# Performance work log

Measured on AMD Instinct MI355X. Metric: run time of the kernel, lower is better.

Reference implementation:

```python
import jax, jax.numpy as jnp
import numpy as np

N = 50000      # nodes
E = 800000     # edges (before self loops)
F_DIM = 512    # raw feature dim
HID = 64       # hidden dim (= per-head dim, concat=False)
HEADS = 4
EMB = 64
NEG_SLOPE = 0.2
LN_EPS = 1e-5


def setup_inputs() -> dict:
    key = jax.random.key(0)
    ks = jax.random.split(key, 24)
    rn = lambda k, shape: jax.random.normal(k, shape, dtype=jnp.float32) * 0.05
    inp = {
        'features': jax.random.normal(ks[0], (N, F_DIM), dtype=jnp.float32),
        'edge_index': jax.random.randint(ks[1], (2, E), 0, N),
        'Wt': rn(ks[2], (F_DIM, HID)), 'bt': jnp.zeros((HID,), jnp.float32),
        'Wp': rn(ks[3], (HID, EMB)), 'bp': jnp.zeros((EMB,), jnp.float32),
    }
    for l in range(2):
        o = 4 + l * 4
        inp[f'Wg{l}'] = rn(ks[o], (HID, HEADS * HID))
        inp[f'as{l}'] = rn(ks[o + 1], (HEADS, HID))
        inp[f'ad{l}'] = rn(ks[o + 2], (HEADS, HID))
        inp[f'bg{l}'] = jnp.zeros((HID,), jnp.float32)
        inp[f'g{l}'] = jnp.ones((HID,), jnp.float32)
        inp[f'b{l}'] = jnp.zeros((HID,), jnp.float32)
        inp[f'a{l}'] = jnp.full((1,), 0.25, jnp.float32)  # PReLU weight
    return inp


def gat_block(x, src, dst, Wg, a_src, a_dst, bg, gamma, beta, prelu_a):
    # GATConv (heads=HEADS, concat=False, add_self_loops already in src/dst)
    h = (x @ Wg).reshape(N, HEADS, HID)                    # [N,H,C]
    al_s = jnp.einsum('nhc,hc->nh', h, a_src)              # [N,H]
    al_d = jnp.einsum('nhc,hc->nh', h, a_dst)
    e = jax.nn.leaky_relu(al_s[src] + al_d[dst], NEG_SLOPE)  # [E,H]
    m = jax.ops.segment_max(e, dst, num_segments=N)
    ex = jnp.exp(e - m[dst])
    denom = jax.ops.segment_sum(ex, dst, num_segments=N)
    alpha = ex / denom[dst]                                # segment softmax over in-edges
    out = jax.ops.segment_sum(h[src] * alpha[:, :, None], dst, num_segments=N)  # [N,H,C]
    out = out.mean(axis=1) + bg                            # concat=False -> mean heads
    # LayerNorm
    mu = out.mean(-1, keepdims=True)
    var = ((out - mu) ** 2).mean(-1, keepdims=True)
    xn = (out - mu) / jnp.sqrt(var + LN_EPS) * gamma + beta
    # PReLU
    return jnp.where(xn > 0, xn, prelu_a * xn)


def reference(features, edge_index, Wt, bt, Wp, bp,
              Wg0, as0, ad0, bg0, g0, b0, a0,
              Wg1, as1, ad1, bg1, g1, b1, a1):
    loops = jnp.arange(N)
    src = jnp.concatenate([edge_index[0], loops])
    dst = jnp.concatenate([edge_index[1], loops])
    x = features @ Wt + bt
    x = x + gat_block(x, src, dst, Wg0, as0, ad0, bg0, g0, b0, a0)
    x = x + gat_block(x, src, dst, Wg1, as1, ad1, bg1, g1, b1, a1)
    z = x @ Wp + bp
    return z / jnp.maximum(jnp.linalg.norm(z, axis=-1, keepdims=True), 1e-12)
```

## Files before the change

### kernel.cpp

```cpp
#include <hip/hip_runtime.h>
#include <hip/hip_bf16.h>

typedef __attribute__((ext_vector_type(8))) short bvec8;
typedef __attribute__((ext_vector_type(4))) float fvec4;

__device__ __forceinline__ void splitf(float f, short& hi, short& lo) {
  __hip_bfloat16 h = __float2bfloat16(f);
  float r = f - __bfloat162float(h);
  __hip_bfloat16 l = __float2bfloat16(r);
  hi = *(short*)&h;
  lo = *(short*)&l;
}
__device__ __forceinline__ float bits2f(unsigned short u) {
  unsigned int v = ((unsigned int)u) << 16;
  return __uint_as_float(v);
}

__global__ void k_degree(const int* __restrict__ ei, int* __restrict__ cnt, int E, int N) {
  int i = blockIdx.x * 256 + threadIdx.x;
  if (i >= E + N) return;
  int d = (i < E) ? ei[E + i] : (i - E);
  atomicAdd(&cnt[d], 1);
}

__global__ __launch_bounds__(1024) void k_scan_blk(const int* __restrict__ cnt, int* __restrict__ off,
                                                   int* __restrict__ bsum, int N) {
  __shared__ int wsum[16];
  int t = threadIdx.x, lane = t & 63, wv = t >> 6;
  int idx = blockIdx.x * 4096 + t * 4;
  int4 v = make_int4(0, 0, 0, 0);
  if (idx < N) v = *(const int4*)(cnt + idx);
  int s0 = v.x, s1 = s0 + v.y, s2 = s1 + v.z, s3 = s2 + v.w;
  int sc = s3;
  #pragma unroll
  for (int d = 1; d < 64; d <<= 1) {
    int u = __shfl_up(sc, d, 64);
    if (lane >= d) sc += u;
  }
  if (lane == 63) wsum[wv] = sc;
  __syncthreads();
  int woff = 0;
  #pragma unroll
  for (int w = 0; w < 16; ++w) woff += (w < wv) ? wsum[w] : 0;
  int eb = woff + sc - s3;
  if (idx < N) {
    int4 o = make_int4(eb, eb + s0, eb + s1, eb + s2);
    *(int4*)(off + idx) = o;
  }
  if (t == 1023) bsum[blockIdx.x] = woff + sc;
}

__global__ __launch_bounds__(1024) void k_scan_add(int* __restrict__ off, int* __restrict__ cur,
                                                   const int* __restrict__ bsum, int total, int N) {
  int t = threadIdx.x;
  if (blockIdx.x == 0 && t == 0) off[N] = total;
  int b = 0;
  for (int i = 0; i < blockIdx.x; ++i) b += bsum[i];
  int idx = blockIdx.x * 4096 + t * 4;
  if (idx >= N) return;
  int4 o = *(const int4*)(off + idx);
  o.x += b; o.y += b; o.z += b; o.w += b;
  *(int4*)(off + idx) = o;
  *(int4*)(cur + idx) = o;
}

__global__ void k_scatter(const int* __restrict__ ei, int* __restrict__ cur, int* __restrict__ csr, int E, int N) {
  int i = blockIdx.x * 256 + threadIdx.x;
  if (i >= E + N) return;
  int s, d;
  if (i < E) { s = ei[i]; d = ei[E + i]; } else { s = i - E; d = i - E; }
  int p = atomicAdd(&cur[d], 1);
  csr[p] = s;
}

__global__ __launch_bounds__(64) void k_prep(const float* __restrict__ Wg0, const float* __restrict__ Wg1,
                                             const float* __restrict__ Wt,
                                             short* __restrict__ pk0, short* __restrict__ pk1,
                                             short* __restrict__ wtpk) {
  int b = blockIdx.x;
  int lane = threadIdx.x;
  int fq = lane >> 4, fr = lane & 15;
  bvec8 hv, lv;
  if (b < 64) {
    const float* Wg = (b < 32) ? Wg0 : Wg1;
    short* pk = (b < 32) ? pk0 : pk1;
    int tile = b & 31;
    int w = tile >> 3, s = (tile >> 2) & 1, ct = tile & 3;
    #pragma unroll
    for (int j = 0; j < 8; ++j) {
      short hh, ll;
      splitf(Wg[(size_t)(s * 32 + fq * 8 + j) * 256 + w * 64 + ct * 16 + fr], hh, ll);
      hv[j] = hh; lv[j] = ll;
    }
    *(bvec8*)(pk + tile * 1024 + lane * 8) = hv;
    *(bvec8*)(pk + tile * 1024 + 512 + lane * 8) = lv;
  } else {
    int tile = b - 64;
    int s = tile >> 2, nt = tile & 3;
    #pragma unroll
    for (int j = 0; j < 8; ++j) {
      short hh, ll;
      splitf(Wt[(size_t)(s * 32 + fq * 8 + j) * 64 + nt * 16 + fr], hh, ll);
      hv[j] = hh; lv[j] = ll;
    }
    *(bvec8*)(wtpk + tile * 1024 + lane * 8) = hv;
    *(bvec8*)(wtpk + tile * 1024 + 512 + lane * 8) = lv;
  }
}

__global__ __launch_bounds__(256) void k_x0(const float* __restrict__ feat, const short* __restrict__ wtpk,
                                            const float* __restrict__ bt,
                                            short* __restrict__ xhi, short* __restrict__ xlo, int N) {
  const int t = threadIdx.x;
  const int lane = t & 63;
  const int w = t >> 6;
  const int fr = lane & 15;
  const int fq = lane >> 4;
  const int n0 = blockIdx.x * 128;

  int ar0 = n0 + w * 32 + fr;      if (ar0 >= N) ar0 = N - 1;
  int ar1 = n0 + w * 32 + 16 + fr; if (ar1 >= N) ar1 = N - 1;
  const float* fb0 = feat + (size_t)ar0 * 512 + fq * 8;
  const float* fb1 = feat + (size_t)ar1 * 512 + fq * 8;

  fvec4 acc[2][4];
  #pragma unroll
  for (int m = 0; m < 2; ++m)
    #pragma unroll
    for (int nt = 0; nt < 4; ++nt) acc[m][nt] = (fvec4){0.f, 0.f, 0.f, 0.f};

  for (int s = 0; s < 16; ++s) {
    bvec8 bh[4], bl[4];
    #pragma unroll
    for (int nt = 0; nt < 4; ++nt) {
      bh[nt] = *(const bvec8*)(wtpk + (s * 4 + nt) * 1024 + lane * 8);
      bl[nt] = *(const bvec8*)(wtpk + (s * 4 + nt) * 1024 + 512 + lane * 8);
    }
    #pragma unroll
    for (int m = 0; m < 2; ++m) {
      const float* fb = m ? fb1 : fb0;
      float4 f0 = *(const float4*)(fb + s * 32);
      float4 f1 = *(const float4*)(fb + s * 32 + 4);
      float fv[8] = {f0.x, f0.y, f0.z, f0.w, f1.x, f1.y, f1.z, f1.w};
      bvec8 ah, al;
      #pragma unroll
      for (int j = 0; j < 8; ++j) { short hh, ll; splitf(fv[j], hh, ll); ah[j] = hh; al[j] = ll; }
      #pragma unroll
      for (int nt = 0; nt < 4; ++nt) {
        acc[m][nt] = __builtin_amdgcn_mfma_f32_16x16x32_bf16(ah, bh[nt], acc[m][nt], 0, 0, 0);
        acc[m][nt] = __builtin_amdgcn_mfma_f32_16x16x32_bf16(ah, bl[nt], acc[m][nt], 0, 0, 0);
        acc[m][nt] = __builtin_amdgcn_mfma_f32_16x16x32_bf16(al, bh[nt], acc[m][nt], 0, 0, 0);
      }
    }
  }
  #pragma unroll
  for (int m = 0; m < 2; ++m)
    #pragma unroll
    for (int nt = 0; nt < 4; ++nt) {
      float btv = bt[nt * 16 + fr];
      #pragma unroll
      for (int r = 0; r < 4; ++r) {
        int node = n0 + w * 32 + m * 16 + fq * 4 + r;
        if (node < N) {
          short hh, ll;
          splitf(acc[m][nt][r] + btv, hh, ll);
          xhi[(size_t)node * 64 + nt * 16 + fr] = hh;
          xlo[(size_t)node * 64 + nt * 16 + fr] = ll;
        }
      }
    }
}

__global__ __launch_bounds__(256) void k_h(const short* __restrict__ xhi, const short* __restrict__ xlo,
                                           const short* __restrict__ pk,
                                           const float* __restrict__ as_, const float* __restrict__ ad_,
                                           signed char* __restrict__ h8, float2* __restrict__ alsc,
                                           float* __restrict__ ald, int N) {
  const int t = threadIdx.x;
  const int lane = t & 63;
  const int w = t >> 6;
  const int fr = lane & 15;
  const int fq = lane >> 4;
  const int n0 = blockIdx.x * 64;

  bvec8 bh[2][4], bl[2][4];
  #pragma unroll
  for (int s = 0; s < 2; ++s)
    #pragma unroll
    for (int ct = 0; ct < 4; ++ct) {
      int tile = (w * 2 + s) * 4 + ct;
      bh[s][ct] = *(const bvec8*)(pk + tile * 1024 + lane * 8);
      bl[s][ct] = *(const bvec8*)(pk + tile * 1024 + 512 + lane * 8);
    }
  fvec4 acc[4][4];
  #pragma unroll
  for (int nt = 0; nt < 4; ++nt)
    #pragma unroll
    for (int ct = 0; ct < 4; ++ct) acc[nt][ct] = (fvec4){0.f, 0.f, 0.f, 0.f};
  #pragma unroll
  for (int nt = 0; nt < 4; ++nt) {
    int row = n0 + nt * 16 + fr; if (row >= N) row = N - 1;
    const short* xh = xhi + (size_t)row * 64 + fq * 8;
    const short* xl = xlo + (size_t)row * 64 + fq * 8;
    #pragma unroll
    for (int s = 0; s < 2; ++s) {
      const bvec8 ah = *(const bvec8*)(xh + s * 32);
      const bvec8 al = *(const bvec8*)(xl + s * 32);
      #pragma unroll
      for (int ct = 0; ct < 4; ++ct) {
        acc[nt][ct] = __builtin_amdgcn_mfma_f32_16x16x32_bf16(ah, bh[s][ct], acc[nt][ct], 0, 0, 0);
        acc[nt][ct] = __builtin_amdgcn_mfma_f32_16x16x32_bf16(ah, bl[s][ct], acc[nt][ct], 0, 0, 0);
        acc[nt][ct] = __builtin_amdgcn_mfma_f32_16x16x32_bf16(al, bh[s][ct], acc[nt][ct], 0, 0, 0);
      }
    }
  }
  float asv[4], adv[4];
  #pragma unroll
  for (int ct = 0; ct < 4; ++ct) {
    asv[ct] = as_[w * 64 + ct * 16 + fr];
    adv[ct] = ad_[w * 64 + ct * 16 + fr];
  }
  #pragma unroll
  for (int nt = 0; nt < 4; ++nt) {
    #pragma unroll
    for (int r = 0; r < 4; ++r) {
      int n = n0 + nt * 16 + fq * 4 + r;
      float ps = 0.f, pd = 0.f;
      float rmax = 0.f;
      #pragma unroll
      for (int ct = 0; ct < 4; ++ct) {
        float av = acc[nt][ct][r];
        ps = fmaf(av, asv[ct], ps);
        pd = fmaf(av, adv[ct], pd);
        rmax = fmaxf(rmax, fabsf(av));
      }
      #pragma unroll
      for (int m = 1; m < 16; m <<= 1) {
        ps += __shfl_xor(ps, m, 64);
        pd += __shfl_xor(pd, m, 64);
        rmax = fmaxf(rmax, __shfl_xor(rmax, m, 64));
      }
      float scale = rmax * (1.f / 127.f);
      float qinv = rmax > 0.f ? 127.f / rmax : 0.f;
      if (fr == 0 && n < N) {
        alsc[(size_t)n * 4 + w] = make_float2(ps, scale);
        ald[(size_t)n * 4 + w] = pd;
      }
      if (n < N) {
        #pragma unroll
        for (int ct = 0; ct < 4; ++ct) {
          int iv = __float2int_rn(acc[nt][ct][r] * qinv);
          h8[(size_t)n * 256 + w * 64 + ct * 16 + fr] = (signed char)iv;
        }
      }
    }
  }
}

template <bool FINAL>
__global__ __launch_bounds__(256) void k_agg(const signed char* __restrict__ h8, const float2* __restrict__ alsc,
                                             const float* __restrict__ ald, const int* __restrict__ off,
                                             const int* __restrict__ csr, const float* __restrict__ bg,
                                             const float* __restrict__ gam, const float* __restrict__ bet,
                                             const float* __restrict__ pa,
                                             short* __restrict__ xhi, short* __restrict__ xlo,
                                             const float* __restrict__ Wp, const float* __restrict__ bp,
                                             float* __restrict__ out, int N) {
  int lane = threadIdx.x & 63;
  int n = blockIdx.x * 4 + (threadIdx.x >> 6);
  if (n >= N) return;
  int hh = lane >> 4;
  int cg = (lane & 15) * 4;
  float aldv = ald[(size_t)n * 4 + hh];
  int e0 = __builtin_amdgcn_readfirstlane(off[n]);
  int e1 = __builtin_amdgcn_readfirstlane(off[n + 1]);
  float a0 = 0, a1 = 0, a2 = 0, a3 = 0, den = 0;
  const int co = hh * 64 + cg;
  int e = e0;
  for (; e + 4 <= e1; e += 4) {
    int s0 = csr[e + 0], s1 = csr[e + 1], s2 = csr[e + 2], s3 = csr[e + 3];
    float2 p0 = alsc[(size_t)s0 * 4 + hh];
    float2 p1 = alsc[(size_t)s1 * 4 + hh];
    float2 p2 = alsc[(size_t)s2 * 4 + hh];
    float2 p3 = alsc[(size_t)s3 * 4 + hh];
    uchar4 g0 = *(const uchar4*)(h8 + (size_t)s0 * 256 + co);
    uchar4 g1 = *(const uchar4*)(h8 + (size_t)s1 * 256 + co);
    uchar4 g2 = *(const uchar4*)(h8 + (size_t)s2 * 256 + co);
    uchar4 g3 = *(const uchar4*)(h8 + (size_t)s3 * 256 + co);
    float t0 = p0.x + aldv; t0 = fmaxf(t0, 0.2f * t0); float w0 = __expf(t0);
    float t1 = p1.x + aldv; t1 = fmaxf(t1, 0.2f * t1); float w1 = __expf(t1);
    float t2 = p2.x + aldv; t2 = fmaxf(t2, 0.2f * t2); float w2 = __expf(t2);
    float t3 = p3.x + aldv; t3 = fmaxf(t3, 0.2f * t3); float w3 = __expf(t3);
    den += (w0 + w1) + (w2 + w3);
    float ws0 = w0 * p0.y, ws1 = w1 * p1.y, ws2 = w2 * p2.y, ws3 = w3 * p3.y;
    a0 += ws0 * (float)(signed char)g0.x + ws1 * (float)(signed char)g1.x
        + ws2 * (float)(signed char)g2.x + ws3 * (float)(signed char)g3.x;
    a1 += ws0 * (float)(signed char)g0.y + ws1 * (float)(signed char)g1.y
        + ws2 * (float)(signed char)g2.y + ws3 * (float)(signed char)g3.y;
    a2 += ws0 * (float)(signed char)g0.z + ws1 * (float)(signed char)g1.z
        + ws2 * (float)(signed char)g2.z + ws3 * (float)(signed char)g3.z;
    a3 += ws0 * (float)(signed char)g0.w + ws1 * (float)(signed char)g1.w
        + ws2 * (float)(signed char)g2.w + ws3 * (float)(signed char)g3.w;
  }
  for (; e < e1; ++e) {
    int s = csr[e];
    float2 p = alsc[(size_t)s * 4 + hh];
    float t = p.x + aldv;
    t = fmaxf(t, 0.2f * t);
    float w = __expf(t);
    den += w;
    float ws = w * p.y;
    uchar4 g = *(const uchar4*)(h8 + (size_t)s * 256 + co);
    a0 += ws * (float)(signed char)g.x;
    a1 += ws * (float)(signed char)g.y;
    a2 += ws * (float)(signed char)g.z;
    a3 += ws * (float)(signed char)g.w;
  }
  float inv = 1.0f / den;
  a0 *= inv; a1 *= inv; a2 *= inv; a3 *= inv;
  a0 += __shfl_xor(a0, 16, 64); a0 += __shfl_xor(a0, 32, 64);
  a1 += __shfl_xor(a1, 16, 64); a1 += __shfl_xor(a1, 32, 64);
  a2 += __shfl_xor(a2, 16, 64); a2 += __shfl_xor(a2, 32, 64);
  a3 += __shfl_xor(a3, 16, 64); a3 += __shfl_xor(a3, 32, 64);
  float v0 = a0 * 0.25f + bg[cg + 0];
  float v1 = a1 * 0.25f + bg[cg + 1];
  float v2 = a2 * 0.25f + bg[cg + 2];
  float v3 = a3 * 0.25f + bg[cg + 3];
  float sum = v0 + v1 + v2 + v3;
  #pragma unroll
  for (int m = 1; m < 16; m <<= 1) sum += __shfl_xor(sum, m, 64);
  float mu = sum * (1.f / 64.f);
  float d0 = v0 - mu, d1 = v1 - mu, d2 = v2 - mu, d3 = v3 - mu;
  float vv = d0 * d0 + d1 * d1 + d2 * d2 + d3 * d3;
  #pragma unroll
  for (int m = 1; m < 16; m <<= 1) vv += __shfl_xor(vv, m, 64);
  float rstd = rsqrtf(vv * (1.f / 64.f) + 1e-5f);
  float A = pa[0];
  float y0 = d0 * rstd * gam[cg + 0] + bet[cg + 0];
  float y1 = d1 * rstd * gam[cg + 1] + bet[cg + 1];
  float y2 = d2 * rstd * gam[cg + 2] + bet[cg + 2];
  float y3 = d3 * rstd * gam[cg + 3] + bet[cg + 3];
  y0 = y0 > 0.f ? y0 : A * y0;
  y1 = y1 > 0.f ? y1 : A * y1;
  y2 = y2 > 0.f ? y2 : A * y2;
  y3 = y3 > 0.f ? y3 : A * y3;
  float o0 = 0.f, o1 = 0.f, o2 = 0.f, o3 = 0.f;
  if (lane < 16) {
    ushort4 xh = *(const ushort4*)((const unsigned short*)xhi + (size_t)n * 64 + cg);
    ushort4 xl = *(const ushort4*)((const unsigned short*)xlo + (size_t)n * 64 + cg);
    o0 = bits2f(xh.x) + bits2f(xl.x) + y0;
    o1 = bits2f(xh.y) + bits2f(xl.y) + y1;
    o2 = bits2f(xh.z) + bits2f(xl.z) + y2;
    o3 = bits2f(xh.w) + bits2f(xl.w) + y3;
  }
  if (!FINAL) {
    if (lane < 16) {
      short h0, l0, h1, l1, h2, l2, h3, l3;
      splitf(o0, h0, l0); splitf(o1, h1, l1); splitf(o2, h2, l2); splitf(o3, h3, l3);
      ushort4 oh = make_ushort4((unsigned short)h0, (unsigned short)h1, (unsigned short)h2, (unsigned short)h3);
      ushort4 ol = make_ushort4((unsigned short)l0, (unsigned short)l1, (unsigned short)l2, (unsigned short)l3);
      *(ushort4*)((unsigned short*)xhi + (size_t)n * 64 + cg) = oh;
      *(ushort4*)((unsigned short*)xlo + (size_t)n * 64 + cg) = ol;
    }
  } else {
    float acc = bp[lane];
    #pragma unroll
    for (int g = 0; g < 16; ++g) {
      float rx = __shfl(o0, g, 64), ry = __shfl(o1, g, 64);
      float rz = __shfl(o2, g, 64), rw = __shfl(o3, g, 64);
      const float* wp = Wp + g * 4 * 64 + lane;
      acc = fmaf(rx, wp[0],   acc);
      acc = fmaf(ry, wp[64],  acc);
      acc = fmaf(rz, wp[128], acc);
      acc = fmaf(rw, wp[192], acc);
    }
    float sq = acc * acc;
    #pragma unroll
    for (int m = 1; m < 64; m <<= 1) sq += __shfl_xor(sq, m, 64);
    float nrm = fmaxf(sqrtf(sq), 1e-12f);
    out[(size_t)n * 64 + lane] = acc / nrm;
  }
}

extern "C" void kernel_launch(void* const* d_in, const int* in_sizes, int n_in,
                              void* d_out, int out_size, void* d_ws, size_t ws_size,
                              hipStream_t stream) {
  const float* feat = (const float*)d_in[0];
  const int*   ei   = (const int*)d_in[1];
  const float* Wt   = (const float*)d_in[2];
  const float* bt   = (const float*)d_in[3];
  const float* Wp   = (const float*)d_in[4];
  const float* bp   = (const float*)d_in[5];
  const float* Wg[2]  = {(const float*)d_in[6],  (const float*)d_in[13]};
  const float* as_[2] = {(const float*)d_in[7],  (const float*)d_in[14]};
  const float* ad_[2] = {(const float*)d_in[8],  (const float*)d_in[15]};
  const float* bg[2]  = {(const float*)d_in[9],  (const float*)d_in[16]};
  const float* gm[2]  = {(const float*)d_in[10], (const float*)d_in[17]};
  const float* be[2]  = {(const float*)d_in[11], (const float*)d_in[18]};
  const float* pa[2]  = {(const float*)d_in[12], (const float*)d_in[19]};

  const int N = in_sizes[0] / 512;
  const int E = in_sizes[1] / 2;

  short* xhi = (short*)d_ws;
  short* xlo = xhi + (size_t)N * 64;
  signed char* h8 = (signed char*)(xlo + (size_t)N * 64);
  float2* alsc = (float2*)(h8 + (size_t)N * 256);
  float* ald = (float*)(alsc + (size_t)N * 4);
  int* cnt = (int*)(ald + (size_t)N * 4);
  int* cur = cnt + N;
  int* csr = cur + N;
  int* off = csr + (E + N);
  int* bsum = off + (N + 1);
  short* pk0 = (short*)(((uintptr_t)(bsum + 16) + 15) & ~(uintptr_t)15);
  short* pk1 = pk0 + 32768;
  short* wtpk = pk1 + 32768;

  hipMemsetAsync(cnt, 0, (size_t)N * sizeof(int), stream);
  int eb = (E + N + 255) / 256;
  int SB = (N + 4095) / 4096;
  k_degree<<<eb, 256, 0, stream>>>(ei, cnt, E, N);
  k_prep<<<128, 64, 0, stream>>>(Wg[0], Wg[1], Wt, pk0, pk1, wtpk);
  k_scan_blk<<<SB, 1024, 0, stream>>>(cnt, off, bsum, N);
  k_scan_add<<<SB, 1024, 0, stream>>>(off, cur, bsum, E + N, N);
  k_scatter<<<eb, 256, 0, stream>>>(ei, cur, csr, E, N);

  int nb4 = (N + 3) / 4;
  int nb64 = (N + 63) / 64;
  int nb128 = (N + 127) / 128;
  k_x0<<<nb128, 256, 0, stream>>>(feat, wtpk, bt, xhi, xlo, N);

  k_h<<<nb64, 256, 0, stream>>>(xhi, xlo, pk0, as_[0], ad_[0], h8, alsc, ald, N);
  k_agg<false><<<nb4, 256, 0, stream>>>(h8, alsc, ald, off, csr, bg[0], gm[0], be[0], pa[0],
                                        xhi, xlo, Wp, bp, (float*)d_out, N);
  k_h<<<nb64, 256, 0, stream>>>(xhi, xlo, pk1, as_[1], ad_[1], h8, alsc, ald, N);
  k_agg<true><<<nb4, 256, 0, stream>>>(h8, alsc, ald, off, csr, bg[1], gm[1], be[1], pa[1],
                                       xhi, xlo, Wp, bp, (float*)d_out, N);
}
```

Baseline: 476.6 us.

## Split edges across lane groups and gather full int8 rows with 16-byte loads

The aggregation kernel's work mapping changes. Each group of 16 lanes now handles a different in-edge and reads a whole 256-byte int8 row with 16-byte vector loads, instead of every lane reading 4 bytes of each edge row in turn. Partial sums are then combined across edge groups and across heads with cross-lane shuffles before LayerNorm, PReLU and the residual. This cuts the number of gather instructions per edge and processes 8 edges per iteration. In exchange, each lane holds 16 accumulators, adds reduction shuffles and a masked tail loop, and the kernel gets a minimum-occupancy hint of 6 blocks.

```diff
diff --git a/kernel.cpp b/kernel.cpp
--- a/kernel.cpp
+++ b/kernel.cpp
@@ -3,6 +3,8 @@
 
 typedef __attribute__((ext_vector_type(8))) short bvec8;
 typedef __attribute__((ext_vector_type(4))) float fvec4;
+typedef __attribute__((ext_vector_type(16))) unsigned char ucvec16;
+typedef __attribute__((ext_vector_type(8))) unsigned short usvec8;
 
 __device__ __forceinline__ void splitf(float f, short& hi, short& lo) {
   __hip_bfloat16 h = __float2bfloat16(f);
@@ -258,121 +260,121 @@
 }
 
 template <bool FINAL>
-__global__ __launch_bounds__(256) void k_agg(const signed char* __restrict__ h8, const float2* __restrict__ alsc,
-                                             const float* __restrict__ ald, const int* __restrict__ off,
-                                             const int* __restrict__ csr, const float* __restrict__ bg,
-                                             const float* __restrict__ gam, const float* __restrict__ bet,
-                                             const float* __restrict__ pa,
-                                             short* __restrict__ xhi, short* __restrict__ xlo,
-                                             const float* __restrict__ Wp, const float* __restrict__ bp,
-                                             float* __restrict__ out, int N) {
-  int lane = threadIdx.x & 63;
-  int n = blockIdx.x * 4 + (threadIdx.x >> 6);
+__global__ __launch_bounds__(256, 6) void k_agg(const signed char* __restrict__ h8, const float2* __restrict__ alsc,
+                                                const float* __restrict__ ald, const int* __restrict__ off,
+                                                const int* __restrict__ csr, const float* __restrict__ bg,
+                                                const float* __restrict__ gam, const float* __restrict__ bet,
+                                                const float* __restrict__ pa,
+                                                short* __restrict__ xhi, short* __restrict__ xlo,
+                                                const float* __restrict__ Wp, const float* __restrict__ bp,
+                                                float* __restrict__ out, int N) {
+  const int lane = threadIdx.x & 63;
+  const int n = blockIdx.x * 4 + (threadIdx.x >> 6);
   if (n >= N) return;
-  int hh = lane >> 4;
-  int cg = (lane & 15) * 4;
-  float aldv = ald[(size_t)n * 4 + hh];
+  const int g = lane >> 4;
+  const int r = lane & 15;
+  const int hd = r >> 2;
+  const int c0 = (r & 3) * 16;
+
+  float aldv = ald[(size_t)n * 4 + hd];
   int e0 = __builtin_amdgcn_readfirstlane(off[n]);
   int e1 = __builtin_amdgcn_readfirstlane(off[n + 1]);
-  float a0 = 0, a1 = 0, a2 = 0, a3 = 0, den = 0;
-  const int co = hh * 64 + cg;
+  float a[16];
+  #pragma unroll
+  for (int k = 0; k < 16; ++k) a[k] = 0.f;
+  float den = 0.f;
+
   int e = e0;
-  for (; e + 4 <= e1; e += 4) {
-    int s0 = csr[e + 0], s1 = csr[e + 1], s2 = csr[e + 2], s3 = csr[e + 3];
-    float2 p0 = alsc[(size_t)s0 * 4 + hh];
-    float2 p1 = alsc[(size_t)s1 * 4 + hh];
-    float2 p2 = alsc[(size_t)s2 * 4 + hh];
-    float2 p3 = alsc[(size_t)s3 * 4 + hh];
-    uchar4 g0 = *(const uchar4*)(h8 + (size_t)s0 * 256 + co);
-    uchar4 g1 = *(const uchar4*)(h8 + (size_t)s1 * 256 + co);
-    uchar4 g2 = *(const uchar4*)(h8 + (size_t)s2 * 256 + co);
-    uchar4 g3 = *(const uchar4*)(h8 + (size_t)s3 * 256 + co);
-    float t0 = p0.x + aldv; t0 = fmaxf(t0, 0.2f * t0); float w0 = __expf(t0);
-    float t1 = p1.x + aldv; t1 = fmaxf(t1, 0.2f * t1); float w1 = __expf(t1);
-    float t2 = p2.x + aldv; t2 = fmaxf(t2, 0.2f * t2); float w2 = __expf(t2);
-    float t3 = p3.x + aldv; t3 = fmaxf(t3, 0.2f * t3); float w3 = __expf(t3);
-    den += (w0 + w1) + (w2 + w3);
-    float ws0 = w0 * p0.y, ws1 = w1 * p1.y, ws2 = w2 * p2.y, ws3 = w3 * p3.y;
-    a0 += ws0 * (float)(signed char)g0.x + ws1 * (float)(signed char)g1.x
-        + ws2 * (float)(signed char)g2.x + ws3 * (float)(signed char)g3.x;
-    a1 += ws0 * (float)(signed char)g0.y + ws1 * (float)(signed char)g1.y
-        + ws2 * (float)(signed char)g2.y + ws3 * (float)(signed char)g3.y;
-    a2 += ws0 * (float)(signed char)g0.z + ws1 * (float)(signed char)g1.z
-        + ws2 * (float)(signed char)g2.z + ws3 * (float)(signed char)g3.z;
-    a3 += ws0 * (float)(signed char)g0.w + ws1 * (float)(signed char)g1.w
-        + ws2 * (float)(signed char)g2.w + ws3 * (float)(signed char)g3.w;
-  }
-  for (; e < e1; ++e) {
-    int s = csr[e];
-    float2 p = alsc[(size_t)s * 4 + hh];
-    float t = p.x + aldv;
-    t = fmaxf(t, 0.2f * t);
-    float w = __expf(t);
+  for (; e + 8 <= e1; e += 8) {
+    int sA = csr[e + g];
+    int sB = csr[e + 4 + g];
+    ucvec16 rowA = *(const ucvec16*)(h8 + (size_t)sA * 256 + r * 16);
+    ucvec16 rowB = *(const ucvec16*)(h8 + (size_t)sB * 256 + r * 16);
+    float2 pA = alsc[(size_t)sA * 4 + hd];
+    float2 pB = alsc[(size_t)sB * 4 + hd];
+    float tA = pA.x + aldv; tA = fmaxf(tA, 0.2f * tA); float wA = __expf(tA);
+    float tB = pB.x + aldv; tB = fmaxf(tB, 0.2f * tB); float wB = __expf(tB);
+    den += wA + wB;
+    float wsA = wA * pA.y, wsB = wB * pB.y;
+    #pragma unroll
+    for (int k = 0; k < 16; ++k) {
+      a[k] = fmaf(wsA, (float)(signed char)rowA[k], a[k]);
+      a[k] = fmaf(wsB, (float)(signed char)rowB[k], a[k]);
+    }
+  }
+  for (; e < e1; e += 4) {
+    int idx = e + g;
+    bool act = idx < e1;
+    int s = csr[act ? idx : (e1 - 1)];
+    ucvec16 row = *(const ucvec16*)(h8 + (size_t)s * 256 + r * 16);
+    float2 p = alsc[(size_t)s * 4 + hd];
+    float t = p.x + aldv; t = fmaxf(t, 0.2f * t);
+    float w = act ? __expf(t) : 0.f;
     den += w;
     float ws = w * p.y;
-    uchar4 g = *(const uchar4*)(h8 + (size_t)s * 256 + co);
-    a0 += ws * (float)(signed char)g.x;
-    a1 += ws * (float)(signed char)g.y;
-    a2 += ws * (float)(signed char)g.z;
-    a3 += ws * (float)(signed char)g.w;
+    #pragma unroll
+    for (int k = 0; k < 16; ++k) a[k] = fmaf(ws, (float)(signed char)row[k], a[k]);
+  }
+
+  den += __shfl_xor(den, 16, 64); den += __shfl_xor(den, 32, 64);
+  #pragma unroll
+  for (int k = 0; k < 16; ++k) {
+    a[k] += __shfl_xor(a[k], 16, 64);
+    a[k] += __shfl_xor(a[k], 32, 64);
   }
   float inv = 1.0f / den;
-  a0 *= inv; a1 *= inv; a2 *= inv; a3 *= inv;
-  a0 += __shfl_xor(a0, 16, 64); a0 += __shfl_xor(a0, 32, 64);
-  a1 += __shfl_xor(a1, 16, 64); a1 += __shfl_xor(a1, 32, 64);
-  a2 += __shfl_xor(a2, 16, 64); a2 += __shfl_xor(a2, 32, 64);
-  a3 += __shfl_xor(a3, 16, 64); a3 += __shfl_xor(a3, 32, 64);
-  float v0 = a0 * 0.25f + bg[cg + 0];
-  float v1 = a1 * 0.25f + bg[cg + 1];
-  float v2 = a2 * 0.25f + bg[cg + 2];
-  float v3 = a3 * 0.25f + bg[cg + 3];
-  float sum = v0 + v1 + v2 + v3;
-  #pragma unroll
-  for (int m = 1; m < 16; m <<= 1) sum += __shfl_xor(sum, m, 64);
-  float mu = sum * (1.f / 64.f);
-  float d0 = v0 - mu, d1 = v1 - mu, d2 = v2 - mu, d3 = v3 - mu;
-  float vv = d0 * d0 + d1 * d1 + d2 * d2 + d3 * d3;
-  #pragma unroll
-  for (int m = 1; m < 16; m <<= 1) vv += __shfl_xor(vv, m, 64);
-  float rstd = rsqrtf(vv * (1.f / 64.f) + 1e-5f);
+  #pragma unroll
+  for (int k = 0; k < 16; ++k) {
+    a[k] *= inv;
+    a[k] += __shfl_xor(a[k], 4, 64);
+    a[k] += __shfl_xor(a[k], 8, 64);
+  }
+  float v[16];
+  float psum = 0.f;
+  #pragma unroll
+  for (int k = 0; k < 16; ++k) {
+    v[k] = a[k] * 0.25f + bg[c0 + k];
+    psum += v[k];
+  }
+  psum += __shfl_xor(psum, 1, 64); psum += __shfl_xor(psum, 2, 64);
+  float mu = psum * (1.f / 64.f);
+  float pvar = 0.f;
+  #pragma unroll
+  for (int k = 0; k < 16; ++k) { float d = v[k] - mu; pvar += d * d; }
+  pvar += __shfl_xor(pvar, 1, 64); pvar += __shfl_xor(pvar, 2, 64);
+  float rstd = rsqrtf(pvar * (1.f / 64.f) + 1e-5f);
   float A = pa[0];
-  float y0 = d0 * rstd * gam[cg + 0] + bet[cg + 0];
-  float y1 = d1 * rstd * gam[cg + 1] + bet[cg + 1];
-  float y2 = d2 * rstd * gam[cg + 2] + bet[cg + 2];
-  float y3 = d3 * rstd * gam[cg + 3] + bet[cg + 3];
-  y0 = y0 > 0.f ? y0 : A * y0;
-  y1 = y1 > 0.f ? y1 : A * y1;
-  y2 = y2 > 0.f ? y2 : A * y2;
-  y3 = y3 > 0.f ? y3 : A * y3;
-  float o0 = 0.f, o1 = 0.f, o2 = 0.f, o3 = 0.f;
-  if (lane < 16) {
-    ushort4 xh = *(const ushort4*)((const unsigned short*)xhi + (size_t)n * 64 + cg);
-    ushort4 xl = *(const ushort4*)((const unsigned short*)xlo + (size_t)n * 64 + cg);
-    o0 = bits2f(xh.x) + bits2f(xl.x) + y0;
-    o1 = bits2f(xh.y) + bits2f(xl.y) + y1;
-    o2 = bits2f(xh.z) + bits2f(xl.z) + y2;
-    o3 = bits2f(xh.w) + bits2f(xl.w) + y3;
+  float o[16];
+  {
+    const unsigned short* xh = (const unsigned short*)xhi + (size_t)n * 64 + c0;
+    const unsigned short* xl = (const unsigned short*)xlo + (size_t)n * 64 + c0;
+    #pragma unroll
+    for (int k = 0; k < 16; ++k) {
+      float y = (v[k] - mu) * rstd * gam[c0 + k] + bet[c0 + k];
+      y = y > 0.f ? y : A * y;
+      o[k] = bits2f(xh[k]) + bits2f(xl[k]) + y;
+    }
   }
   if (!FINAL) {
-    if (lane < 16) {
-      short h0, l0, h1, l1, h2, l2, h3, l3;
-      splitf(o0, h0, l0); splitf(o1, h1, l1); splitf(o2, h2, l2); splitf(o3, h3, l3);
-      ushort4 oh = make_ushort4((unsigned short)h0, (unsigned short)h1, (unsigned short)h2, (unsigned short)h3);
-      ushort4 ol = make_ushort4((unsigned short)l0, (unsigned short)l1, (unsigned short)l2, (unsigned short)l3);
-      *(ushort4*)((unsigned short*)xhi + (size_t)n * 64 + cg) = oh;
-      *(ushort4*)((unsigned short*)xlo + (size_t)n * 64 + cg) = ol;
+    if (lane < 4) {
+      unsigned short oh[16], ol[16];
+      #pragma unroll
+      for (int k = 0; k < 16; ++k) {
+        short hh, ll; splitf(o[k], hh, ll);
+        oh[k] = (unsigned short)hh; ol[k] = (unsigned short)ll;
+      }
+      #pragma unroll
+      for (int q = 0; q < 2; ++q) {
+        *(usvec8*)((unsigned short*)xhi + (size_t)n * 64 + c0 + q * 8) = *(usvec8*)(oh + q * 8);
+        *(usvec8*)((unsigned short*)xlo + (size_t)n * 64 + c0 + q * 8) = *(usvec8*)(ol + q * 8);
+      }
     }
   } else {
     float acc = bp[lane];
     #pragma unroll
-    for (int g = 0; g < 16; ++g) {
-      float rx = __shfl(o0, g, 64), ry = __shfl(o1, g, 64);
-      float rz = __shfl(o2, g, 64), rw = __shfl(o3, g, 64);
-      const float* wp = Wp + g * 4 * 64 + lane;
-      acc = fmaf(rx, wp[0],   acc);
-      acc = fmaf(ry, wp[64],  acc);
-      acc = fmaf(rz, wp[128], acc);
-      acc = fmaf(rw, wp[192], acc);
+    for (int c = 0; c < 64; ++c) {
+      float val = __shfl(o[c & 15], c >> 4, 64);
+      acc = fmaf(val, Wp[c * 64 + lane], acc);
     }
     float sq = acc * acc;
     #pragma unroll
```

After: 505.9 us. 6.1% more time.
